# Kernel optimization log

Hardware: AMD Instinct MI355X
Metric: run time of the kernel (lower is better)

## Reference

```python
import jax, jax.numpy as jnp
import numpy as np

B, S, D, H = 2, 2048, 1024, 16
HD = D // H


def setup_inputs() -> dict:
    key = jax.random.key(0)
    ks = jax.random.split(key, 16)
    sc = 0.02
    return {
        "hidden_states": jax.random.normal(ks[0], (B, S, D), jnp.float32),
        "Wq": jax.random.normal(ks[1], (D, D), jnp.float32) * sc,
        "bq": jnp.zeros((D,), jnp.float32),
        "Wk": jax.random.normal(ks[2], (D, D), jnp.float32) * sc,
        "bk": jnp.zeros((D,), jnp.float32),
        "Wv": jax.random.normal(ks[3], (D, D), jnp.float32) * sc,
        "bv": jnp.zeros((D,), jnp.float32),
        "Wo": jax.random.normal(ks[4], (D, D), jnp.float32) * sc,
        "bo": jnp.zeros((D,), jnp.float32),
        "rel_W": jax.random.normal(ks[5], (3, 2 * D), jnp.float32) * sc,
        "rel_b": jnp.zeros((3,), jnp.float32),
        "logical_bias": jax.random.normal(ks[6], (H, 3), jnp.float32) * sc,
        "gate_W": jax.random.normal(ks[7], (H, D), jnp.float32) * sc,
        "gate_b": jnp.zeros((H,), jnp.float32),
    }


def reference(hidden_states, Wq, bq, Wk, bk, Wv, bv, Wo, bo,
              rel_W, rel_b, logical_bias, gate_W, gate_b):
    x = hidden_states
    b, s, d = x.shape
    h = gate_W.shape[0]
    hd = d // h
    scale = hd ** 0.5

    q = (x @ Wq.T + bq).reshape(b, s, h, hd)
    k = (x @ Wk.T + bk).reshape(b, s, h, hd)
    v = (x @ Wv.T + bv).reshape(b, s, h, hd)

    # [b, h, i, j] raw attention scores
    attn_scores = jnp.einsum('bihd,bjhd->bhij', q, k) / scale

    # Pairwise relation logits WITHOUT materializing the [b,s,s,2d] concat:
    # cat([h_i, h_j]) @ W.T == h_i @ W[:, :d].T + h_j @ W[:, d:].T
    li = x @ rel_W[:, :d].T   # (b, s, 3) contribution from position i
    lj = x @ rel_W[:, d:].T   # (b, s, 3) contribution from position j
    logits = li[:, :, None, :] + lj[:, None, :, :] + rel_b  # (b, s, s, 3)
    relation_probs = jax.nn.softmax(logits, axis=-1)

    bias = jnp.einsum('bijk,hk->bhij', relation_probs, logical_bias)

    gate = jax.nn.sigmoid(x @ gate_W.T + gate_b)        # (b, s, h)
    gate = jnp.transpose(gate, (0, 2, 1))[..., None]    # (b, h, s, 1)

    attn_scores = attn_scores + gate * bias
    attn_weights = jax.nn.softmax(attn_scores, axis=-1)

    out = jnp.einsum('bhij,bjhd->bihd', attn_weights, v).reshape(b, s, d)
    return out @ Wo.T + bo
```

## Files before the change

### kernel.cpp

```cpp
#include <hip/hip_runtime.h>
#include <math.h>

#define B_   2
#define S_   2048
#define D_   1024
#define H_   16
#define NROW (B_ * S_)
#define L2E_ 1.4426950408889634f

typedef __bf16 bf16_t;
typedef __bf16 bf16x8 __attribute__((ext_vector_type(8)));
typedef __bf16 bf16x4v __attribute__((ext_vector_type(4)));
typedef float  f32x4  __attribute__((ext_vector_type(4)));

#define MFMA16(a, b, c) __builtin_amdgcn_mfma_f32_16x16x32_bf16((a), (b), (c), 0, 0, 0)

#if __has_builtin(__builtin_amdgcn_exp2f)
#define EXP2F(x) __builtin_amdgcn_exp2f(x)
#else
#define EXP2F(x) exp2f(x)
#endif

__device__ __forceinline__ void glds16(const void* src, void* lds) {
    __builtin_amdgcn_global_load_lds(
        (const __attribute__((address_space(1))) void*)src,
        (__attribute__((address_space(3))) void*)lds, 16, 0, 0);
}

__global__ __launch_bounds__(256)
void cvt_all(const float* __restrict__ x, const float* __restrict__ wq,
             const float* __restrict__ wk, const float* __restrict__ wv,
             const float* __restrict__ wo, bf16_t* __restrict__ xb,
             bf16_t* __restrict__ wqb, bf16_t* __restrict__ wkb,
             bf16_t* __restrict__ wvb, bf16_t* __restrict__ wob) {
    int bid = blockIdx.x;
    const float* src;
    bf16_t* dst;
    int base;
    if (bid < 4096) { src = x; dst = xb; base = bid; }
    else {
        int k = (bid - 4096) >> 10;
        base = (bid - 4096) & 1023;
        src = (k == 0) ? wq : (k == 1) ? wk : (k == 2) ? wv : wo;
        dst = (k == 0) ? wqb : (k == 1) ? wkb : (k == 2) ? wvb : wob;
    }
    int idx = base * 1024 + threadIdx.x * 4;
    float4 v = *(const float4*)&src[idx];
    bf16x4v o;
    o[0] = (bf16_t)v.x; o[1] = (bf16_t)v.y; o[2] = (bf16_t)v.z; o[3] = (bf16_t)v.w;
    *(bf16x4v*)&dst[idx] = o;
}

__global__ __launch_bounds__(256)
void proj_small(const float* __restrict__ x, const float* __restrict__ relW,
                const float* __restrict__ relB, const float* __restrict__ gateW,
                const float* __restrict__ gateB,
                float* __restrict__ EA4, float* __restrict__ EB4,
                float* __restrict__ GA) {
    const int wave = threadIdx.x >> 6;
    const int lane = threadIdx.x & 63;
    const int row  = blockIdx.x * 4 + wave;

    const float4* xr = (const float4*)(x + (size_t)row * D_);
    float4 xv[4];
    #pragma unroll
    for (int t = 0; t < 4; ++t) xv[t] = xr[lane + 64 * t];

    for (int c = 0; c < 22; ++c) {
        const float* w;
        if (c < 3)       w = relW + c * (2 * D_);
        else if (c < 6)  w = relW + (c - 3) * (2 * D_) + D_;
        else             w = gateW + (size_t)(c - 6) * D_;
        const float4* w4 = (const float4*)w;
        float s = 0.f;
        #pragma unroll
        for (int t = 0; t < 4; ++t) {
            float4 wv = w4[lane + 64 * t];
            s += xv[t].x * wv.x + xv[t].y * wv.y + xv[t].z * wv.z + xv[t].w * wv.w;
        }
        #pragma unroll
        for (int off = 32; off; off >>= 1) s += __shfl_xor(s, off);
        if (lane == 0) {
            if (c < 3)      EA4[row * 4 + c] = expf(s + relB[c]);
            else if (c < 6) EB4[row * 4 + (c - 3)] = expf(s);
            else            GA[row * H_ + (c - 6)] =
                                1.f / (1.f + expf(-(s + gateB[c - 6])));
        }
    }
}

__device__ __forceinline__ void gemm_body128(
    const bf16_t* __restrict__ A, const bf16_t* __restrict__ W,
    const float* __restrict__ bias, float scale, int row0, int col0,
    bf16_t* As, bf16_t* Bs, int outbf16, void* Cout, int N, int K)
{
    const int tid = threadIdx.x, w = tid >> 6, l = tid & 63;
    const int wr = w >> 1, wc = w & 1, p16 = l & 15, g4 = l >> 4;

    f32x4 acc[4][4];
    #pragma unroll
    for (int i = 0; i < 4; ++i)
        #pragma unroll
        for (int j = 0; j < 4; ++j) acc[i][j] = (f32x4){0.f, 0.f, 0.f, 0.f};

    const int sr = l >> 3, sc = l & 7;
    const bf16_t* aS = A + (size_t)(row0 + w * 32) * K;
    const bf16_t* bS = W + (size_t)(col0 + w * 32) * K;

    for (int k0 = 0; k0 < K; k0 += 64) {
        #pragma unroll
        for (int i = 0; i < 4; ++i) {
            int r = i * 8 + sr;
            int co = k0 + ((sc ^ sr) << 3);
            glds16(aS + (size_t)r * K + co, As + (w * 32 + i * 8) * 64);
            glds16(bS + (size_t)r * K + co, Bs + (w * 32 + i * 8) * 64);
        }
        __syncthreads();
        #pragma unroll
        for (int c = 0; c < 2; ++c) {
            bf16x8 af[4], bfr[4];
            #pragma unroll
            for (int mi = 0; mi < 4; ++mi) {
                int row = wr * 64 + mi * 16 + p16;
                af[mi] = *(const bf16x8*)&As[row * 64 + (((c * 4 + g4) ^ (row & 7)) << 3)];
            }
            #pragma unroll
            for (int nj = 0; nj < 4; ++nj) {
                int row = wc * 64 + nj * 16 + p16;
                bfr[nj] = *(const bf16x8*)&Bs[row * 64 + (((c * 4 + g4) ^ (row & 7)) << 3)];
            }
            #pragma unroll
            for (int mi = 0; mi < 4; ++mi)
                #pragma unroll
                for (int nj = 0; nj < 4; ++nj)
                    acc[mi][nj] = MFMA16(af[mi], bfr[nj], acc[mi][nj]);
        }
        __syncthreads();
    }

    const int cj = col0 + wc * 64 + p16;
    #pragma unroll
    for (int nj = 0; nj < 4; ++nj) {
        int j = cj + nj * 16;
        float bj = bias[j];
        #pragma unroll
        for (int mi = 0; mi < 4; ++mi) {
            int ib = row0 + wr * 64 + mi * 16 + g4 * 4;
            #pragma unroll
            for (int r = 0; r < 4; ++r) {
                float v = (acc[mi][nj][r] + bj) * scale;
                if (outbf16)
                    ((bf16_t*)Cout)[(size_t)(ib + r) * N + j] = (bf16_t)v;
                else
                    ((float*)Cout)[(size_t)(ib + r) * N + j] = v;
            }
        }
    }
}

__global__ __launch_bounds__(256)
void gemm_qkv(const bf16_t* __restrict__ xb,
              const bf16_t* __restrict__ wq, const bf16_t* __restrict__ wk,
              const bf16_t* __restrict__ wv,
              const float* __restrict__ bq, const float* __restrict__ bk,
              const float* __restrict__ bv,
              bf16_t* __restrict__ Qb, bf16_t* __restrict__ Kb,
              bf16_t* __restrict__ Vb) {
    __shared__ __align__(16) bf16_t As[128 * 64];
    __shared__ __align__(16) bf16_t Bs[128 * 64];
    const int seg = blockIdx.x >> 3;
    const int col0 = (blockIdx.x & 7) * 128;
    const int row0 = blockIdx.y * 128;
    const bf16_t* W = (seg == 0) ? wq : (seg == 1) ? wk : wv;
    const float* bias = (seg == 0) ? bq : (seg == 1) ? bk : bv;
    bf16_t* C = (seg == 0) ? Qb : (seg == 1) ? Kb : Vb;
    const float scale = (seg == 0) ? 0.125f * L2E_ : 1.0f;
    gemm_body128(xb, W, bias, scale, row0, col0, As, Bs, 1, C, D_, D_);
}

__global__ __launch_bounds__(256)
void gemm_out(const bf16_t* __restrict__ A, const bf16_t* __restrict__ wo,
              const float* __restrict__ bo, float* __restrict__ out) {
    __shared__ __align__(16) bf16_t As[128 * 64];
    __shared__ __align__(16) bf16_t Bs[128 * 64];
    gemm_body128(A, wo, bo, 1.0f, blockIdx.y * 128, blockIdx.x * 128,
                 As, Bs, 0, out, D_, D_);
}

__global__ __launch_bounds__(256, 3)
void flash_mfma(const bf16_t* __restrict__ Q, const bf16_t* __restrict__ Kg,
                const bf16_t* __restrict__ Vg, const float4* __restrict__ EA4,
                const float4* __restrict__ EB4, const float* __restrict__ GA,
                const float* __restrict__ LB, bf16_t* __restrict__ AO) {
    __shared__ __align__(16) bf16_t Ks[2][4096];
    __shared__ __align__(16) bf16_t Vt[2][4096];
    __shared__ __align__(16) bf16_t Ps[4][1024];
    __shared__ __align__(16) float  ebs[2][256];

    const int tid = threadIdx.x, w = tid >> 6, l = tid & 63;
    const int b = blockIdx.y >> 4, h = blockIdx.y & 15;
    const int i0 = blockIdx.x * 64;
    const size_t rowb = (size_t)b * S_ + i0;
    const int p16 = l & 15, g4 = l >> 4;

    const float lb0 = LB[h * 3 + 0], lb1 = LB[h * 3 + 1], lb2 = LB[h * 3 + 2];

    bf16x8 qf[2];
    {
        const bf16_t* qp = Q + (rowb + w * 16 + p16) * D_ + h * 64 + g4 * 8;
        qf[0] = *(const bf16x8*)qp;
        qf[1] = *(const bf16x8*)(qp + 32);
    }

    bf16x8 zer;
    #pragma unroll
    for (int u = 0; u < 8; ++u) zer[u] = (bf16_t)0.f;
    bf16x8 cnf = zer, eaf = zer;
    {
        size_t gi = rowb + w * 16 + p16;
        float4 e = EA4[gi];
        float g = GA[gi * H_ + h] * L2E_;
        if (g4 == 0) {
            cnf[0] = (bf16_t)(g * e.x * lb0);
            cnf[1] = (bf16_t)(g * e.y * lb1);
            cnf[2] = (bf16_t)(g * e.z * lb2);
            eaf[0] = (bf16_t)e.x;
            eaf[1] = (bf16_t)e.y;
            eaf[2] = (bf16_t)e.z;
        }
    }

    const int vj = tid >> 2, vc = (tid & 3) * 16;
    const int kr0 = l >> 3, kc0 = l & 7;
    const size_t koff1 = (size_t)(w * 16 + kr0) * D_ + ((kc0 ^ kr0) << 3);
    const size_t koff2 = koff1 + 8 * D_;

    bf16x8 v0, v1;
    float4 ebr;

#define LOADV(jt) do {                                                         \
        const size_t jb0 = (size_t)b * S_ + (jt);                              \
        const bf16_t* vp = Vg + (jb0 + vj) * D_ + h * 64 + vc;                 \
        v0 = *(const bf16x8*)vp;                                               \
        v1 = *(const bf16x8*)(vp + 8);                                         \
        if (tid < 64) ebr = EB4[jb0 + tid];                                    \
    } while (0)

#define WRITEV(buf) do {                                                       \
        _Pragma("unroll")                                                      \
        for (int u = 0; u < 8; ++u) {                                          \
            int hd = vc + u;                                                   \
            int sw = ((hd & 7) ^ ((hd >> 3) & 7)) << 3;                        \
            Vt[buf][hd * 64 + (vj ^ sw)] = v0[u];                              \
        }                                                                      \
        _Pragma("unroll")                                                      \
        for (int u = 0; u < 8; ++u) {                                          \
            int hd = vc + 8 + u;                                               \
            int sw = ((hd & 7) ^ ((hd >> 3) & 7)) << 3;                        \
            Vt[buf][hd * 64 + (vj ^ sw)] = v1[u];                              \
        }                                                                      \
        if (tid < 64) *(float4*)&ebs[buf][tid * 4] = ebr;                      \
    } while (0)

#define STAGEK(buf, jt) do {                                                   \
        const size_t jbase = (size_t)(b * S_ + (jt)) * D_ + h * 64;            \
        glds16(Kg + jbase + koff1, &Ks[buf][w * 1024]);                        \
        glds16(Kg + jbase + koff2, &Ks[buf][w * 1024 + 512]);                  \
    } while (0)

    float lsum[4] = {0.f, 0.f, 0.f, 0.f};
    f32x4 o[4];
    #pragma unroll
    for (int nb = 0; nb < 4; ++nb) o[nb] = (f32x4){0.f, 0.f, 0.f, 0.f};

    LOADV(0);
    STAGEK(0, 0);
    WRITEV(0);
    LOADV(64);
    __syncthreads();

    for (int t = 0; t < 32; ++t) {
        const int cur = t & 1;
        if (t < 31) { WRITEV(cur ^ 1); STAGEK(cur ^ 1, (t + 1) * 64); }
        if (t < 30) LOADV((t + 2) * 64);

        f32x4 nacc[4], dacc[4];
        #pragma unroll
        for (int nb = 0; nb < 4; ++nb) {
            float4 e = *(const float4*)&ebs[cur][(nb * 16 + p16) * 4];
            bf16x8 ebf = zer;
            if (g4 == 0) {
                ebf[0] = (bf16_t)e.x; ebf[1] = (bf16_t)e.y; ebf[2] = (bf16_t)e.z;
            }
            f32x4 z4 = (f32x4){0.f, 0.f, 0.f, 0.f};
            nacc[nb] = MFMA16(cnf, ebf, z4);
            dacc[nb] = MFMA16(eaf, ebf, z4);
        }

        f32x4 s[4];
        #pragma unroll
        for (int nb = 0; nb < 4; ++nb) {
            s[nb] = (f32x4){0.f, 0.f, 0.f, 0.f};
            int row = nb * 16 + p16;
            int sw = row & 7;
            bf16x8 k0v = *(const bf16x8*)&Ks[cur][row * 64 + ((g4    ) ^ sw) * 8];
            bf16x8 k1v = *(const bf16x8*)&Ks[cur][row * 64 + ((g4 + 4) ^ sw) * 8];
            s[nb] = MFMA16(qf[0], k0v, s[nb]);
            s[nb] = MFMA16(qf[1], k1v, s[nb]);
        }

        #pragma unroll
        for (int nb = 0; nb < 4; ++nb) {
            #pragma unroll
            for (int r = 0; r < 4; ++r) {
                float sv = s[nb][r] + nacc[nb][r] * __builtin_amdgcn_rcpf(dacc[nb][r]);
                float p = EXP2F(sv);
                bf16_t pb = (bf16_t)p;
                lsum[r] += (float)pb;
                int irow = g4 * 4 + r;
                int jcol = nb * 16 + p16;
                Ps[w][irow * 64 + (jcol ^ ((irow & 7) << 3))] = pb;
            }
        }

        bf16x8 pf0, pf1;
        {
            int sw = p16 & 7;
            pf0 = *(const bf16x8*)&Ps[w][p16 * 64 + ((g4    ) ^ sw) * 8];
            pf1 = *(const bf16x8*)&Ps[w][p16 * 64 + ((g4 + 4) ^ sw) * 8];
        }
        #pragma unroll
        for (int nb = 0; nb < 4; ++nb) {
            int vrow = nb * 16 + p16;
            int sw = (vrow & 7) ^ ((vrow >> 3) & 7);
            bf16x8 vf0 = *(const bf16x8*)&Vt[cur][vrow * 64 + ((g4    ) ^ sw) * 8];
            bf16x8 vf1 = *(const bf16x8*)&Vt[cur][vrow * 64 + ((g4 + 4) ^ sw) * 8];
            o[nb] = MFMA16(pf0, vf0, o[nb]);
            o[nb] = MFMA16(pf1, vf1, o[nb]);
        }
        __syncthreads();
    }
#undef LOADV
#undef WRITEV
#undef STAGEK

    #pragma unroll
    for (int r = 0; r < 4; ++r) {
        float t = lsum[r];
        t += __shfl_xor(t, 1); t += __shfl_xor(t, 2);
        t += __shfl_xor(t, 4); t += __shfl_xor(t, 8);
        lsum[r] = 1.f / t;
    }
    #pragma unroll
    for (int nb = 0; nb < 4; ++nb)
        #pragma unroll
        for (int r = 0; r < 4; ++r) {
            size_t gi = rowb + w * 16 + g4 * 4 + r;
            AO[gi * D_ + h * 64 + nb * 16 + p16] = (bf16_t)(o[nb][r] * lsum[r]);
        }
}

extern "C" void kernel_launch(void* const* d_in, const int* in_sizes, int n_in,
                              void* d_out, int out_size, void* d_ws, size_t ws_size,
                              hipStream_t stream) {
    const float* x    = (const float*)d_in[0];
    const float* Wq   = (const float*)d_in[1];
    const float* bq   = (const float*)d_in[2];
    const float* Wk   = (const float*)d_in[3];
    const float* bk   = (const float*)d_in[4];
    const float* Wv   = (const float*)d_in[5];
    const float* bv   = (const float*)d_in[6];
    const float* Wo   = (const float*)d_in[7];
    const float* bo   = (const float*)d_in[8];
    const float* relW = (const float*)d_in[9];
    const float* relB = (const float*)d_in[10];
    const float* lb   = (const float*)d_in[11];
    const float* gW   = (const float*)d_in[12];
    const float* gb   = (const float*)d_in[13];

    uint8_t* W8 = (uint8_t*)d_ws;
    bf16_t* xb  = (bf16_t*)(W8);
    bf16_t* wqb = (bf16_t*)(W8 + (8u  << 20));
    bf16_t* wkb = (bf16_t*)(W8 + (10u << 20));
    bf16_t* wvb = (bf16_t*)(W8 + (12u << 20));
    bf16_t* wob = (bf16_t*)(W8 + (14u << 20));
    bf16_t* Qb  = (bf16_t*)(W8 + (16u << 20));
    bf16_t* Kb  = (bf16_t*)(W8 + (24u << 20));
    bf16_t* Vb  = (bf16_t*)(W8 + (32u << 20));
    bf16_t* AOb = (bf16_t*)(W8 + (40u << 20));
    float*  EA  = (float*)(W8 + (48u << 20));
    float*  EB  = (float*)(W8 + (48u << 20) + 65536);
    float*  GAp = (float*)(W8 + (48u << 20) + 131072);

    cvt_all<<<8192, 256, 0, stream>>>(x, Wq, Wk, Wv, Wo, xb, wqb, wkb, wvb, wob);
    proj_small<<<NROW / 4, 256, 0, stream>>>(x, relW, relB, gW, gb, EA, EB, GAp);

    gemm_qkv<<<dim3(24, 32), 256, 0, stream>>>(xb, wqb, wkb, wvb, bq, bk, bv,
                                               Qb, Kb, Vb);

    flash_mfma<<<dim3(S_ / 64, B_ * H_), 256, 0, stream>>>(
        Qb, Kb, Vb, (const float4*)EA, (const float4*)EB, GAp, lb, AOb);

    gemm_out<<<dim3(8, 32), 256, 0, stream>>>(AOb, wob, bo, (float*)d_out);
}
```

Baseline: 281.6 us.

## Write V transposed from QKV GEMM and stage K/V via direct LDS loads

Measured after the change: 270.0 us. -4.1%, faster.

```diff
diff --git a/kernel.cpp b/kernel.cpp
--- a/kernel.cpp
+++ b/kernel.cpp
@@ -12,6 +12,8 @@
 typedef __bf16 bf16x8 __attribute__((ext_vector_type(8)));
 typedef __bf16 bf16x4v __attribute__((ext_vector_type(4)));
 typedef float  f32x4  __attribute__((ext_vector_type(4)));
+typedef unsigned u32x2 __attribute__((ext_vector_type(2)));
+typedef unsigned u32x4 __attribute__((ext_vector_type(4)));
 
 #define MFMA16(a, b, c) __builtin_amdgcn_mfma_f32_16x16x32_bf16((a), (b), (c), 0, 0, 0)
 
@@ -55,7 +57,7 @@
 void proj_small(const float* __restrict__ x, const float* __restrict__ relW,
                 const float* __restrict__ relB, const float* __restrict__ gateW,
                 const float* __restrict__ gateB,
-                float* __restrict__ EA4, float* __restrict__ EB4,
+                float* __restrict__ EA4, bf16_t* __restrict__ EBb,
                 float* __restrict__ GA) {
     const int wave = threadIdx.x >> 6;
     const int lane = threadIdx.x & 63;
@@ -82,8 +84,10 @@
         for (int off = 32; off; off >>= 1) s += __shfl_xor(s, off);
         if (lane == 0) {
             if (c < 3)      EA4[row * 4 + c] = expf(s + relB[c]);
-            else if (c < 6) EB4[row * 4 + (c - 3)] = expf(s);
-            else            GA[row * H_ + (c - 6)] =
+            else if (c < 6) {
+                EBb[row * 4 + (c - 3)] = (bf16_t)expf(s);
+                if (c == 5) EBb[row * 4 + 3] = (bf16_t)0.f;
+            } else          GA[row * H_ + (c - 6)] =
                                 1.f / (1.f + expf(-(s + gateB[c - 6])));
         }
     }
@@ -92,7 +96,8 @@
 __device__ __forceinline__ void gemm_body128(
     const bf16_t* __restrict__ A, const bf16_t* __restrict__ W,
     const float* __restrict__ bias, float scale, int row0, int col0,
-    bf16_t* As, bf16_t* Bs, int outbf16, void* Cout, int N, int K)
+    bf16_t* As, bf16_t* Bs, int outbf16, void* Cout,
+    size_t csI, size_t csJ, int K)
 {
     const int tid = threadIdx.x, w = tid >> 6, l = tid & 63;
     const int wr = w >> 1, wc = w & 1, p16 = l & 15, g4 = l >> 4;
@@ -149,10 +154,11 @@
             #pragma unroll
             for (int r = 0; r < 4; ++r) {
                 float v = (acc[mi][nj][r] + bj) * scale;
+                size_t addr = (size_t)(ib + r) * csI + (size_t)j * csJ;
                 if (outbf16)
-                    ((bf16_t*)Cout)[(size_t)(ib + r) * N + j] = (bf16_t)v;
+                    ((bf16_t*)Cout)[addr] = (bf16_t)v;
                 else
-                    ((float*)Cout)[(size_t)(ib + r) * N + j] = v;
+                    ((float*)Cout)[addr] = v;
             }
         }
     }
@@ -165,7 +171,7 @@
               const float* __restrict__ bq, const float* __restrict__ bk,
               const float* __restrict__ bv,
               bf16_t* __restrict__ Qb, bf16_t* __restrict__ Kb,
-              bf16_t* __restrict__ Vb) {
+              bf16_t* __restrict__ Vtb) {
     __shared__ __align__(16) bf16_t As[128 * 64];
     __shared__ __align__(16) bf16_t Bs[128 * 64];
     const int seg = blockIdx.x >> 3;
@@ -173,9 +179,11 @@
     const int row0 = blockIdx.y * 128;
     const bf16_t* W = (seg == 0) ? wq : (seg == 1) ? wk : wv;
     const float* bias = (seg == 0) ? bq : (seg == 1) ? bk : bv;
-    bf16_t* C = (seg == 0) ? Qb : (seg == 1) ? Kb : Vb;
+    bf16_t* C = (seg == 0) ? Qb : (seg == 1) ? Kb : Vtb;
     const float scale = (seg == 0) ? 0.125f * L2E_ : 1.0f;
-    gemm_body128(xb, W, bias, scale, row0, col0, As, Bs, 1, C, D_, D_);
+    const size_t csI = (seg == 2) ? 1 : (size_t)D_;
+    const size_t csJ = (seg == 2) ? (size_t)NROW : 1;
+    gemm_body128(xb, W, bias, scale, row0, col0, As, Bs, 1, C, csI, csJ, D_);
 }
 
 __global__ __launch_bounds__(256)
@@ -184,18 +192,17 @@
     __shared__ __align__(16) bf16_t As[128 * 64];
     __shared__ __align__(16) bf16_t Bs[128 * 64];
     gemm_body128(A, wo, bo, 1.0f, blockIdx.y * 128, blockIdx.x * 128,
-                 As, Bs, 0, out, D_, D_);
-}
-
-__global__ __launch_bounds__(256, 3)
+                 As, Bs, 0, out, (size_t)D_, 1, D_);
+}
+
+__global__ __launch_bounds__(256, 4)
 void flash_mfma(const bf16_t* __restrict__ Q, const bf16_t* __restrict__ Kg,
-                const bf16_t* __restrict__ Vg, const float4* __restrict__ EA4,
-                const float4* __restrict__ EB4, const float* __restrict__ GA,
+                const bf16_t* __restrict__ Vtg, const float4* __restrict__ EA4,
+                const bf16_t* __restrict__ EBb, const float* __restrict__ GA,
                 const float* __restrict__ LB, bf16_t* __restrict__ AO) {
     __shared__ __align__(16) bf16_t Ks[2][4096];
-    __shared__ __align__(16) bf16_t Vt[2][4096];
+    __shared__ __align__(16) bf16_t Vs[2][4096];
     __shared__ __align__(16) bf16_t Ps[4][1024];
-    __shared__ __align__(16) float  ebs[2][256];
 
     const int tid = threadIdx.x, w = tid >> 6, l = tid & 63;
     const int b = blockIdx.y >> 4, h = blockIdx.y & 15;
@@ -230,42 +237,18 @@
         }
     }
 
-    const int vj = tid >> 2, vc = (tid & 3) * 16;
     const int kr0 = l >> 3, kc0 = l & 7;
-    const size_t koff1 = (size_t)(w * 16 + kr0) * D_ + ((kc0 ^ kr0) << 3);
-    const size_t koff2 = koff1 + 8 * D_;
-
-    bf16x8 v0, v1;
-    float4 ebr;
-
-#define LOADV(jt) do {                                                         \
-        const size_t jb0 = (size_t)b * S_ + (jt);                              \
-        const bf16_t* vp = Vg + (jb0 + vj) * D_ + h * 64 + vc;                 \
-        v0 = *(const bf16x8*)vp;                                               \
-        v1 = *(const bf16x8*)(vp + 8);                                         \
-        if (tid < 64) ebr = EB4[jb0 + tid];                                    \
-    } while (0)
-
-#define WRITEV(buf) do {                                                       \
-        _Pragma("unroll")                                                      \
-        for (int u = 0; u < 8; ++u) {                                          \
-            int hd = vc + u;                                                   \
-            int sw = ((hd & 7) ^ ((hd >> 3) & 7)) << 3;                        \
-            Vt[buf][hd * 64 + (vj ^ sw)] = v0[u];                              \
-        }                                                                      \
-        _Pragma("unroll")                                                      \
-        for (int u = 0; u < 8; ++u) {                                          \
-            int hd = vc + 8 + u;                                               \
-            int sw = ((hd & 7) ^ ((hd >> 3) & 7)) << 3;                        \
-            Vt[buf][hd * 64 + (vj ^ sw)] = v1[u];                              \
-        }                                                                      \
-        if (tid < 64) *(float4*)&ebs[buf][tid * 4] = ebr;                      \
-    } while (0)
-
-#define STAGEK(buf, jt) do {                                                   \
-        const size_t jbase = (size_t)(b * S_ + (jt)) * D_ + h * 64;            \
-        glds16(Kg + jbase + koff1, &Ks[buf][w * 1024]);                        \
-        glds16(Kg + jbase + koff2, &Ks[buf][w * 1024 + 512]);                  \
+    const int rowA = w * 16 + kr0, rowB = rowA + 8;
+    const bf16_t* KpA = Kg + ((size_t)b * S_ + rowA) * D_ + h * 64 + ((kc0 ^ (rowA & 7)) << 3);
+    const bf16_t* KpB = Kg + ((size_t)b * S_ + rowB) * D_ + h * 64 + ((kc0 ^ (rowB & 7)) << 3);
+    const bf16_t* VpA = Vtg + (size_t)(h * 64 + rowA) * NROW + (size_t)b * S_ + ((kc0 ^ (rowA & 7)) << 3);
+    const bf16_t* VpB = Vtg + (size_t)(h * 64 + rowB) * NROW + (size_t)b * S_ + ((kc0 ^ (rowB & 7)) << 3);
+
+#define STAGE(buf, jt) do {                                                    \
+        glds16(KpA + (size_t)(jt) * D_, &Ks[buf][w * 1024]);                   \
+        glds16(KpB + (size_t)(jt) * D_, &Ks[buf][w * 1024 + 512]);             \
+        glds16(VpA + (jt), &Vs[buf][w * 1024]);                                \
+        glds16(VpB + (jt), &Vs[buf][w * 1024 + 512]);                          \
     } while (0)
 
     float lsum[4] = {0.f, 0.f, 0.f, 0.f};
@@ -273,29 +256,23 @@
     #pragma unroll
     for (int nb = 0; nb < 4; ++nb) o[nb] = (f32x4){0.f, 0.f, 0.f, 0.f};
 
-    LOADV(0);
-    STAGEK(0, 0);
-    WRITEV(0);
-    LOADV(64);
+    STAGE(0, 0);
     __syncthreads();
+
+    const bf16_t* ebbase = EBb + (size_t)b * S_ * 4;
 
     for (int t = 0; t < 32; ++t) {
         const int cur = t & 1;
-        if (t < 31) { WRITEV(cur ^ 1); STAGEK(cur ^ 1, (t + 1) * 64); }
-        if (t < 30) LOADV((t + 2) * 64);
-
-        f32x4 nacc[4], dacc[4];
-        #pragma unroll
-        for (int nb = 0; nb < 4; ++nb) {
-            float4 e = *(const float4*)&ebs[cur][(nb * 16 + p16) * 4];
-            bf16x8 ebf = zer;
-            if (g4 == 0) {
-                ebf[0] = (bf16_t)e.x; ebf[1] = (bf16_t)e.y; ebf[2] = (bf16_t)e.z;
-            }
-            f32x4 z4 = (f32x4){0.f, 0.f, 0.f, 0.f};
-            nacc[nb] = MFMA16(cnf, ebf, z4);
-            dacc[nb] = MFMA16(eaf, ebf, z4);
-        }
+
+        u32x2 ebl[4];
+        {
+            const bf16_t* ebp = ebbase + (size_t)t * 64 * 4;
+            #pragma unroll
+            for (int nb = 0; nb < 4; ++nb)
+                ebl[nb] = *(const u32x2*)&ebp[(nb * 16 + p16) * 4];
+        }
+
+        if (t < 31) STAGE(cur ^ 1, (t + 1) * 64);
 
         f32x4 s[4];
         #pragma unroll
@@ -304,9 +281,19 @@
             int row = nb * 16 + p16;
             int sw = row & 7;
             bf16x8 k0v = *(const bf16x8*)&Ks[cur][row * 64 + ((g4    ) ^ sw) * 8];
-            bf16x8 k1v = *(const bf16x8*)&Ks[cur][row * 64 + ((g4 + 4) ^ sw) * 8];
+            bf16x8 k1v = *(const bf16x8*)&Ks[cur][row * 64 + (((g4 + 4)) ^ sw) * 8];
             s[nb] = MFMA16(qf[0], k0v, s[nb]);
             s[nb] = MFMA16(qf[1], k1v, s[nb]);
+        }
+
+        f32x4 nacc[4], dacc[4];
+        #pragma unroll
+        for (int nb = 0; nb < 4; ++nb) {
+            u32x4 uu = {g4 == 0 ? ebl[nb][0] : 0u, g4 == 0 ? ebl[nb][1] : 0u, 0u, 0u};
+            bf16x8 ebf = __builtin_bit_cast(bf16x8, uu);
+            f32x4 z4 = (f32x4){0.f, 0.f, 0.f, 0.f};
+            nacc[nb] = MFMA16(cnf, ebf, z4);
+            dacc[nb] = MFMA16(eaf, ebf, z4);
         }
 
         #pragma unroll
@@ -332,17 +319,15 @@
         #pragma unroll
         for (int nb = 0; nb < 4; ++nb) {
             int vrow = nb * 16 + p16;
-            int sw = (vrow & 7) ^ ((vrow >> 3) & 7);
-            bf16x8 vf0 = *(const bf16x8*)&Vt[cur][vrow * 64 + ((g4    ) ^ sw) * 8];
-            bf16x8 vf1 = *(const bf16x8*)&Vt[cur][vrow * 64 + ((g4 + 4) ^ sw) * 8];
+            int sw = vrow & 7;
+            bf16x8 vf0 = *(const bf16x8*)&Vs[cur][vrow * 64 + ((g4    ) ^ sw) * 8];
+            bf16x8 vf1 = *(const bf16x8*)&Vs[cur][vrow * 64 + ((g4 + 4) ^ sw) * 8];
             o[nb] = MFMA16(pf0, vf0, o[nb]);
             o[nb] = MFMA16(pf1, vf1, o[nb]);
         }
         __syncthreads();
     }
-#undef LOADV
-#undef WRITEV
-#undef STAGEK
+#undef STAGE
 
     #pragma unroll
     for (int r = 0; r < 4; ++r) {
@@ -386,20 +371,20 @@
     bf16_t* wob = (bf16_t*)(W8 + (14u << 20));
     bf16_t* Qb  = (bf16_t*)(W8 + (16u << 20));
     bf16_t* Kb  = (bf16_t*)(W8 + (24u << 20));
-    bf16_t* Vb  = (bf16_t*)(W8 + (32u << 20));
+    bf16_t* Vtb = (bf16_t*)(W8 + (32u << 20));
     bf16_t* AOb = (bf16_t*)(W8 + (40u << 20));
     float*  EA  = (float*)(W8 + (48u << 20));
-    float*  EB  = (float*)(W8 + (48u << 20) + 65536);
-    float*  GAp = (float*)(W8 + (48u << 20) + 131072);
+    bf16_t* EBb = (bf16_t*)(W8 + (48u << 20) + 65536);
+    float*  GAp = (float*)(W8 + (48u << 20) + 98304);
 
     cvt_all<<<8192, 256, 0, stream>>>(x, Wq, Wk, Wv, Wo, xb, wqb, wkb, wvb, wob);
-    proj_small<<<NROW / 4, 256, 0, stream>>>(x, relW, relB, gW, gb, EA, EB, GAp);
+    proj_small<<<NROW / 4, 256, 0, stream>>>(x, relW, relB, gW, gb, EA, EBb, GAp);
 
     gemm_qkv<<<dim3(24, 32), 256, 0, stream>>>(xb, wqb, wkb, wvb, bq, bk, bv,
-                                               Qb, Kb, Vb);
+                                               Qb, Kb, Vtb);
 
     flash_mfma<<<dim3(S_ / 64, B_ * H_), 256, 0, stream>>>(
-        Qb, Kb, Vb, (const float4*)EA, (const float4*)EB, GAp, lb, AOb);
+        Qb, Kb, Vtb, (const float4*)EA, EBb, GAp, lb, AOb);
 
     gemm_out<<<dim3(8, 32), 256, 0, stream>>>(AOb, wob, bo, (float*)d_out);
 }
```
